# Kernel optimization log

Measured on AMD Instinct MI355X. Metric: run time of the kernel, lower is better.

## Reference

```python
import jax, jax.numpy as jnp
import numpy as np

# graph sizes: G graphs of N_PER nodes each (block-diagonal batched graph)
G, N_PER, F, NHID, E_PER = 128, 512, 128, 128, 4096
N = G * N_PER
E = G * E_PER
L1, L2, L3 = 4, 2, 2            # PANConv filter sizes (conv1 uses init filter_size=4)
K1, K2, K3 = N_PER // 2, N_PER // 4, N_PER // 8  # ratio=0.5 top-k per pooling stage


def setup_inputs() -> dict:
    ks = jax.random.split(jax.random.key(0), 10)
    rng = np.random.default_rng(0)
    off = (np.arange(G) * N_PER)[:, None]
    src = (rng.integers(0, N_PER, size=(G, E_PER)) + off).reshape(-1)
    dst = (rng.integers(0, N_PER, size=(G, E_PER)) + off).reshape(-1)
    edge_index = jnp.asarray(np.stack([src, dst]).astype(np.int32))
    batch = jnp.repeat(jnp.arange(G, dtype=jnp.int32), N_PER)
    def w(k, shp, fan):
        return jax.random.normal(k, shp, jnp.float32) / np.float32(np.sqrt(fan))
    z = lambda *s: jnp.zeros(s, jnp.float32)
    return dict(
        x=jax.random.normal(ks[0], (N, F), jnp.float32),
        edge_index=edge_index, batch=batch,
        lump_W=w(ks[1], (F, NHID), F), lump_b=z(NHID),
        conv1_W=w(ks[2], (NHID, NHID), NHID), conv1_b=z(NHID),
        conv2_W=w(ks[3], (NHID, NHID), NHID), conv2_b=z(NHID),
        conv3_W=w(ks[4], (NHID, NHID), NHID), conv3_b=z(NHID),
        pool1_p=w(ks[5], (NHID,), NHID), pool1_beta=jnp.full((2,), 0.5, jnp.float32),
        pool2_p=w(ks[6], (NHID,), NHID), pool2_beta=jnp.full((2,), 0.5, jnp.float32),
        pool3_p=w(ks[7], (NHID,), NHID), pool3_beta=jnp.full((2,), 0.5, jnp.float32),
        lin1_W=w(ks[8], (NHID, NHID // 2), NHID), lin1_b=z(NHID // 2),
        lin2_W=w(ks[9], (NHID // 2, 1), NHID // 2), lin2_b=z(1),
    )


def _pan_prop(h, src, dst, ew, L):
    # (sum_{l=0..L} A^l) @ h, A weighted by edge weights ew, via iterated gather/scatter
    acc, y = h, h
    n = h.shape[0]
    for _ in range(L):
        y = jax.ops.segment_sum(y[src] * ew[:, None], dst, num_segments=n)
        acc = acc + y
    return acc


def _pan_conv(x, src, dst, ew, W, b, L):
    # PANConv: M = Z^{-1/2} (sum_{l<=L} A^l) Z^{-1/2};  out = M x W + b
    d = _pan_prop(jnp.ones((x.shape[0], 1), x.dtype), src, dst, ew, L)[:, 0]
    dinv = jax.lax.rsqrt(jnp.maximum(d, 1e-12))
    h = dinv[:, None] * _pan_prop(dinv[:, None] * x, src, dst, ew, L)
    return h @ W + b


def _pan_pool(x, src, dst, ew, p, beta, n_per, k):
    # PANPooling: score = beta0*(x.p)/||p|| + beta1*node_strength; per-graph top-k
    n = x.shape[0]
    deg = jax.ops.segment_sum(ew, dst, num_segments=n)
    score = beta[0] * (x @ p) / jnp.linalg.norm(p) + beta[1] * deg
    _, idx = jax.lax.top_k(score.reshape(G, n_per), k)          # [G, k] local indices
    perm = (idx + (jnp.arange(G) * n_per)[:, None]).reshape(-1)  # [G*k] global
    x_new = x[perm] * jnp.tanh(score[perm])[:, None]
    inv = jnp.zeros((n,), jnp.int32).at[perm].set(jnp.arange(G * k, dtype=jnp.int32))
    mask = jnp.zeros((n,), x.dtype).at[perm].set(1.0)
    # keep edge arrays fixed-size: dropped edges get weight 0 (same math as filtering)
    return x_new, inv[src], inv[dst], ew * mask[src] * mask[dst], perm


def reference(x, edge_index, batch, lump_W, lump_b, conv1_W, conv1_b, conv2_W, conv2_b,
              conv3_W, conv3_b, pool1_p, pool1_beta, pool2_p, pool2_beta, pool3_p,
              pool3_beta, lin1_W, lin1_b, lin2_W, lin2_b):
    src, dst = edge_index[0], edge_index[1]
    ew = jnp.ones((src.shape[0],), x.dtype)
    h = x @ lump_W + lump_b                                   # PANLump lift
    h = _pan_conv(h, src, dst, ew, conv1_W, conv1_b, L1)
    h, src, dst, ew, perm1 = _pan_pool(h, src, dst, ew, pool1_p, pool1_beta, N_PER, K1)
    h = _pan_conv(h, src, dst, ew, conv2_W, conv2_b, L2)
    h, src, dst, ew, perm2 = _pan_pool(h, src, dst, ew, pool2_p, pool2_beta, K1, K2)
    h = _pan_conv(h, src, dst, ew, conv3_W, conv3_b, L3)
    h, src, dst, ew, perm3 = _pan_pool(h, src, dst, ew, pool3_p, pool3_beta, K2, K3)
    seg = jnp.repeat(jnp.arange(G, dtype=jnp.int32), K3)
    mean = jax.ops.segment_sum(h, seg, num_segments=G) / jnp.float32(K3)  # scatter_mean
    out = jax.nn.relu(mean @ lin1_W + lin1_b) @ lin2_W + lin2_b           # [G, 1]
    return out
```

## Files before the change

### kernel.cpp

```cpp
#include <hip/hip_runtime.h>
#include <math.h>

#define G_     128
#define E_     524288
#define EPG    4096
#define DEGMAX 48

typedef __attribute__((ext_vector_type(8))) short bf16x8;
typedef __attribute__((ext_vector_type(4))) float f32x4;
typedef __attribute__((ext_vector_type(4))) unsigned short u16x4;

__device__ inline void split_bf16(float x, short& hi, short& lo){
    unsigned u = __float_as_uint(x);
    hi = (short)(u >> 16);
    float hf = __uint_as_float(u & 0xffff0000u);
    unsigned r = __float_as_uint(x - hf);
    lo = (short)(r >> 16);
}

__device__ inline int ysw(int v, int f4){ return v*32 + (f4 ^ ((v & 7) << 2)); }

template<int WAVES>
__device__ void gemm_body(char* smem, int bid, const float* __restrict__ X,
        const float* __restrict__ W, const float* __restrict__ bias, float* __restrict__ Y,
        const float* __restrict__ p, const float* __restrict__ beta,
        const int* __restrict__ cntv, float* __restrict__ score){
    short* wsh = (short*)smem;
    short* wsl = (short*)(smem + 34816);
    float* bsh = (float*)(smem + 69632);
    float* qs  = (float*)(smem + 70144);
    float* rednorm = (float*)(smem + 70656);
    const int NT = WAVES*64;
    int t = threadIdx.x;
    for (int e = t; e < 16384; e += NT){
        int k = e >> 7, n = e & 127;
        short hi, lo; split_bf16(W[e], hi, lo);
        wsh[n*136 + k] = hi; wsl[n*136 + k] = lo;
    }
    if (t < 128) bsh[t] = bias[t];
    if (score && t < 64){ float a = p[t], b = p[t+64]; rednorm[t] = a*a + b*b; }
    __syncthreads();
    float b1 = 0.f;
    if (score){
        if (t == 0){ float s = 0.f; for (int i = 0; i < 64; i++) s += rednorm[i]; rednorm[0] = sqrtf(s); }
        __syncthreads();
        if (t < 128) qs[t] = beta[0] * p[t] / rednorm[0];
        b1 = beta[1];
        __syncthreads();
    }
    int wave = t >> 6, lane = t & 63;
    int ln = lane & 15, q = lane >> 4;
    size_t rb = (size_t)bid * (WAVES*16);
    const float* xrow = &X[(rb + wave*16 + ln)*128 + q*8];
    f32x4 acc[8];
    #pragma unroll
    for (int i = 0; i < 8; i++) acc[i] = (f32x4){0.f,0.f,0.f,0.f};
    #pragma unroll
    for (int kc = 0; kc < 4; kc++){
        float4 xa = *(const float4*)(xrow + kc*32);
        float4 xb = *(const float4*)(xrow + kc*32 + 4);
        bf16x8 ah, al; short hi, lo;
        split_bf16(xa.x, hi, lo); ah[0]=hi; al[0]=lo;
        split_bf16(xa.y, hi, lo); ah[1]=hi; al[1]=lo;
        split_bf16(xa.z, hi, lo); ah[2]=hi; al[2]=lo;
        split_bf16(xa.w, hi, lo); ah[3]=hi; al[3]=lo;
        split_bf16(xb.x, hi, lo); ah[4]=hi; al[4]=lo;
        split_bf16(xb.y, hi, lo); ah[5]=hi; al[5]=lo;
        split_bf16(xb.z, hi, lo); ah[6]=hi; al[6]=lo;
        split_bf16(xb.w, hi, lo); ah[7]=hi; al[7]=lo;
        #pragma unroll
        for (int nt = 0; nt < 8; nt++){
            int wo = (nt*16 + ln)*136 + kc*32 + q*8;
            bf16x8 bh = *(const bf16x8*)&wsh[wo];
            bf16x8 bl = *(const bf16x8*)&wsl[wo];
            acc[nt] = __builtin_amdgcn_mfma_f32_16x16x32_bf16(ah, bh, acc[nt], 0, 0, 0);
            acc[nt] = __builtin_amdgcn_mfma_f32_16x16x32_bf16(ah, bl, acc[nt], 0, 0, 0);
            acc[nt] = __builtin_amdgcn_mfma_f32_16x16x32_bf16(al, bh, acc[nt], 0, 0, 0);
        }
    }
    #pragma unroll
    for (int nt = 0; nt < 8; nt++){
        int c = nt*16 + ln;
        float bb = bsh[c];
        #pragma unroll
        for (int r = 0; r < 4; r++){
            Y[(rb + wave*16 + q*4 + r)*128 + c] = acc[nt][r] + bb;
        }
    }
    if (score){
        #pragma unroll
        for (int r = 0; r < 4; r++){
            float sp = 0.f;
            #pragma unroll
            for (int nt = 0; nt < 8; nt++){
                int c = nt*16 + ln;
                sp += (acc[nt][r] + bsh[c]) * qs[c];
            }
            sp += __shfl_xor(sp, 1);
            sp += __shfl_xor(sp, 2);
            sp += __shfl_xor(sp, 4);
            sp += __shfl_xor(sp, 8);
            if (ln == 0){
                int row = (int)rb + wave*16 + q*4 + r;
                score[row] = sp + b1 * (float)cntv[row];
            }
        }
    }
}

template<int WAVES>
__global__ __launch_bounds__(WAVES*64) void k_gemm_mfma(const float* __restrict__ X,
        const float* __restrict__ W, const float* __restrict__ bias, float* __restrict__ Y,
        const float* __restrict__ p, const float* __restrict__ beta,
        const int* __restrict__ cntv, float* __restrict__ score){
    __shared__ __align__(16) char smem[70912];
    gemm_body<WAVES>(smem, blockIdx.x, X, W, bias, Y, p, beta, cntv, score);
}

__global__ __launch_bounds__(512) void k_prep1(const int* __restrict__ ei,
        int* __restrict__ cnt, unsigned short* __restrict__ csrcp,
        int* __restrict__ permg, float* __restrict__ dinvg){
    __shared__ int   lcnt[512];
    __shared__ __align__(16) unsigned short csrS[512*DEGMAX + 8];
    __shared__ float y[1024];
    __shared__ int   bins[64];
    __shared__ int   permS[512];
    int g = blockIdx.x, t = threadIdx.x, gbase = g*512;
    lcnt[t] = 0;
    if (t < 64) bins[t] = 0;
    unsigned* c32 = (unsigned*)csrS;
    for (int i = t; i < 512*DEGMAX/2 + 4; i += 512) c32[i] = 0;
    __syncthreads();
    for (int i = t; i < EPG; i += 512){
        int e = g*EPG + i;
        int sv = ei[e] & 511;
        int d  = ei[E_ + e] & 511;
        int slot = atomicAdd(&lcnt[d], 1);
        if (slot < DEGMAX) csrS[d*DEGMAX + slot] = (unsigned short)sv;
    }
    __syncthreads();
    {
        unsigned* dst = (unsigned*)(csrcp + (size_t)gbase*DEGMAX);
        for (int i = t; i < 512*DEGMAX/2; i += 512) dst[i] = c32[i];
    }
    int rawc = lcnt[t];
    cnt[gbase + t] = rawc;
    int dc = min(rawc, DEGMAX);
    atomicAdd(&bins[dc], 1);
    __syncthreads();
    if (t < 64){
        int v0 = bins[t], s = v0;
        #pragma unroll
        for (int off = 1; off < 64; off <<= 1){
            int n = __shfl_up(s, off);
            if (t >= off) s += n;
        }
        bins[t] = s - v0;
    }
    __syncthreads();
    {
        int slot = atomicAdd(&bins[dc], 1);
        int pk = t | (dc << 16);
        permS[slot] = pk;
        permg[gbase + slot] = pk;
    }
    __syncthreads();
    int pk = permS[t];
    int pv = pk & 0xffff, pd = pk >> 16;
    y[pv] = 1.f;
    __syncthreads();
    float dacc = 1.f;
    int cur = 0;
    for (int l = 0; l < 4; l++){
        const float* la = &y[cur*512];
        float s = 0.f;
        int nq = (pd + 3) >> 2;
        const u16x4* cp = (const u16x4*)(csrS + pv*DEGMAX);
        u16x4 oc = cp[0];
        #pragma unroll 1
        for (int jq = 0; jq < nq; jq++){
            u16x4 ocn = cp[jq + 1];
            s += (la[(int)oc[0]] + la[(int)oc[1]]) + (la[(int)oc[2]] + la[(int)oc[3]]);
            oc = ocn;
        }
        if (nq) s -= (float)(nq*4 - pd) * la[0];
        y[(1^cur)*512 + pv] = s;
        dacc += s;
        __syncthreads();
        cur ^= 1;
    }
    dinvg[gbase + pv] = rsqrtf(fmaxf(dacc, 1e-12f));
}

template<int NPER, int L, int IT, bool SEL>
__global__ __launch_bounds__(1024)
void k_prop(const int* __restrict__ permg, const float* __restrict__ dinvg,
        const unsigned short* __restrict__ csrcp,
        const float* __restrict__ X, const int* __restrict__ selg,
        const float* __restrict__ thg, float* __restrict__ OUT){
    __shared__ __align__(16) float y[NPER*32];
    __shared__ float dinvs[NPER];
    int g = blockIdx.x, fq = blockIdx.y, gbase = g*NPER;
    int t = threadIdx.x;
    int f4 = (t & 7)*4;
    int fo = fq*32 + f4;
    if (t < NPER) dinvs[t] = dinvg[gbase + t];
    int pkr[IT];
    {
        int wv = t >> 6, gi = (t >> 3) & 7;
        #pragma unroll
        for (int it = 0; it < IT; it++){
            int ch = (it & 1) ? (15 - wv) : wv;
            pkr[it] = permg[gbase + (16*it + ch)*8 + gi];
        }
    }
    __syncthreads();
    float4 acc[IT];
    #pragma unroll
    for (int it = 0; it < IT; it++){
        int v = pkr[it] & 0xffff;
        float d = dinvs[v];
        size_t row;
        if (SEL){
            row = (size_t)selg[gbase + v];
            d *= thg[gbase + v];
        } else {
            row = (size_t)(gbase + v);
        }
        float4 w = *(const float4*)&X[row*128 + fo];
        w.x*=d; w.y*=d; w.z*=d; w.w*=d;
        acc[it] = w;
        *(float4*)&y[ysw(v, f4)] = w;
    }
    __syncthreads();
    for (int l = 0; l < L; l++){
        float4 s[IT];
        #pragma unroll
        for (int it = 0; it < IT; it++){
            int pk = pkr[it];
            int c = pk >> 16;
            int nq = (c + 3) >> 2;
            const u16x4* cp = (const u16x4*)(csrcp + (size_t)(gbase + (pk & 0xffff))*DEGMAX);
            float4 ss = make_float4(0.f,0.f,0.f,0.f);
            u16x4 oc = cp[0];
            #pragma unroll 1
            for (int jq = 0; jq < nq; jq++){
                u16x4 ocn = cp[jq + 1];
                float4 w0 = *(const float4*)&y[ysw((int)oc[0], f4)];
                float4 w1 = *(const float4*)&y[ysw((int)oc[1], f4)];
                float4 w2 = *(const float4*)&y[ysw((int)oc[2], f4)];
                float4 w3 = *(const float4*)&y[ysw((int)oc[3], f4)];
                ss.x += (w0.x + w1.x) + (w2.x + w3.x);
                ss.y += (w0.y + w1.y) + (w2.y + w3.y);
                ss.z += (w0.z + w1.z) + (w2.z + w3.z);
                ss.w += (w0.w + w1.w) + (w2.w + w3.w);
                oc = ocn;
            }
            if (nq){
                float fp = (float)(nq*4 - c);
                float4 z = *(const float4*)&y[f4];
                ss.x -= fp*z.x; ss.y -= fp*z.y; ss.z -= fp*z.z; ss.w -= fp*z.w;
            }
            s[it] = ss;
        }
        __syncthreads();
        #pragma unroll
        for (int it = 0; it < IT; it++){
            int v = pkr[it] & 0xffff;
            *(float4*)&y[ysw(v, f4)] = s[it];
            acc[it].x+=s[it].x; acc[it].y+=s[it].y; acc[it].z+=s[it].z; acc[it].w+=s[it].w;
        }
        __syncthreads();
    }
    #pragma unroll
    for (int it = 0; it < IT; it++){
        int v = pkr[it] & 0xffff;
        float d = dinvs[v];
        float4 w = acc[it];
        w.x*=d; w.y*=d; w.z*=d; w.w*=d;
        *(float4*)&OUT[(size_t)(gbase + v)*128 + fo] = w;
    }
}

template<int NPER, bool BUILD>
__global__ __launch_bounds__(512) void k_pooltop(const float* __restrict__ score_in,
        const int* __restrict__ esrc_in, const int* __restrict__ edst_in,
        int* __restrict__ esrc_out, int* __restrict__ edst_out,
        int* __restrict__ cnt_next, unsigned short* __restrict__ csrcp,
        int* __restrict__ permg, float* __restrict__ dinvg,
        int* __restrict__ selg, float* __restrict__ thg){
    const int K = NPER/2;
    constexpr int CSRSZ = BUILD ? (NPER/2)*DEGMAX + 8 : 8;
    __shared__ __align__(16) float sc[NPER];
    __shared__ int  nid[NPER];
    __shared__ int  lcnt[NPER/2];
    __shared__ int  bins[64];
    __shared__ int  permS[NPER/2];
    __shared__ __align__(16) unsigned short csrS[CSRSZ];
    int g = blockIdx.x, t = threadIdx.x, gbase = g*NPER;
    if (t < K) lcnt[t] = 0;
    if (t < 64) bins[t] = 0;
    if (BUILD){
        unsigned* c32 = (unsigned*)csrS;
        for (int i = t; i < K*DEGMAX/2 + 4; i += 512) c32[i] = 0;
    }
    if (t < NPER) sc[t] = score_in[gbase + t];
    __syncthreads();
    if (t < NPER){
        float s = sc[t];
        int rank = 0;
        const float4* sc4 = (const float4*)sc;
        #pragma unroll 8
        for (int j4 = 0; j4 < NPER/4; j4++){
            float4 v = sc4[j4];
            int j = j4*4;
            rank += (v.x > s) || (v.x == s && (j+0) < t);
            rank += (v.y > s) || (v.y == s && (j+1) < t);
            rank += (v.z > s) || (v.z == s && (j+2) < t);
            rank += (v.w > s) || (v.w == s && (j+3) < t);
        }
        if (rank < K){
            nid[t] = g*K + rank;
            selg[g*K + rank] = gbase + t;
            thg[g*K + rank]  = tanhf(s);
        } else nid[t] = -1;
    }
    __syncthreads();
    if (BUILD){
        for (int i = t; i < EPG; i += 512){
            int e = g*EPG + i;
            int d = edst_in[e];
            if (d < 0) continue;
            int s_ = esrc_in[e];
            int ns = nid[s_ - gbase], nd = nid[d - gbase];
            if ((ns | nd) < 0){ edst_out[e] = -1; }
            else {
                esrc_out[e] = ns; edst_out[e] = nd;
                int ndl = nd & (K-1);
                int slot = atomicAdd(&lcnt[ndl], 1);
                if (slot < DEGMAX) csrS[ndl*DEGMAX + slot] = (unsigned short)(ns & (K-1));
            }
        }
        __syncthreads();
        {
            unsigned* c32 = (unsigned*)csrS;
            unsigned* dst = (unsigned*)(csrcp + (size_t)g*K*DEGMAX);
            for (int i = t; i < K*DEGMAX/2; i += 512) dst[i] = c32[i];
        }
        float* yd = sc;
        int rawc = 0, dc = 0;
        if (t < K){
            rawc = lcnt[t];
            cnt_next[g*K + t] = rawc;
            dc = min(rawc, DEGMAX);
            atomicAdd(&bins[dc], 1);
        }
        __syncthreads();
        if (t < 64){
            int v0 = bins[t], s = v0;
            #pragma unroll
            for (int off = 1; off < 64; off <<= 1){
                int n = __shfl_up(s, off);
                if (t >= off) s += n;
            }
            bins[t] = s - v0;
        }
        __syncthreads();
        if (t < K){
            int slot = atomicAdd(&bins[dc], 1);
            permS[slot] = t | (dc << 16);
            permg[g*K + slot] = permS[slot];
        }
        __syncthreads();
        int pv = 0, pd = 0;
        if (t < K){
            int pk = permS[t];
            pv = pk & 0xffff; pd = pk >> 16;
            yd[pv] = 1.f;
        }
        __syncthreads();
        float dacc = 1.f;
        int cur = 0;
        for (int l = 0; l < 2; l++){
            if (t < K){
                const float* la = &yd[cur*K];
                float s = 0.f;
                int nq = (pd + 3) >> 2;
                const u16x4* cp = (const u16x4*)(csrS + pv*DEGMAX);
                u16x4 oc = cp[0];
                #pragma unroll 1
                for (int jq = 0; jq < nq; jq++){
                    u16x4 ocn = cp[jq + 1];
                    s += (la[(int)oc[0]] + la[(int)oc[1]]) + (la[(int)oc[2]] + la[(int)oc[3]]);
                    oc = ocn;
                }
                if (nq) s -= (float)(nq*4 - pd) * la[0];
                yd[(1^cur)*K + pv] = s;
                dacc += s;
            }
            __syncthreads();
            cur ^= 1;
        }
        if (t < K) dinvg[g*K + pv] = rsqrtf(fmaxf(dacc, 1e-12f));
    }
}

__global__ __launch_bounds__(512) void k_stage3(const float* __restrict__ X,
        const float* __restrict__ W, const float* __restrict__ bias,
        const float* __restrict__ p, const float* __restrict__ beta,
        const int* __restrict__ cntv,
        const float* __restrict__ W1, const float* __restrict__ b1,
        const float* __restrict__ W2, const float* __restrict__ b2,
        float* __restrict__ out){
    __shared__ __align__(16) char smem[70912];
    __shared__ float scs[128];
    __shared__ float thS[64];
    __shared__ int   selS[64];
    __shared__ float mr[128];
    short* wsh = (short*)smem;
    short* wsl = (short*)(smem + 34816);
    float* bsh = (float*)(smem + 69632);
    float* qs  = (float*)(smem + 70144);
    float* rednorm = (float*)(smem + 70656);
    int g = blockIdx.x, t = threadIdx.x;
    for (int e = t; e < 16384; e += 512){
        int k = e >> 7, n = e & 127;
        short hi, lo; split_bf16(W[e], hi, lo);
        wsh[n*136 + k] = hi; wsl[n*136 + k] = lo;
    }
    if (t < 128) bsh[t] = bias[t];
    if (t < 64){ float a = p[t], b = p[t+64]; rednorm[t] = a*a + b*b; }
    __syncthreads();
    if (t == 0){ float s = 0.f; for (int i = 0; i < 64; i++) s += rednorm[i]; rednorm[0] = sqrtf(s); }
    __syncthreads();
    if (t < 128) qs[t] = beta[0] * p[t] / rednorm[0];
    float b1v = beta[1];
    __syncthreads();
    int wave = t >> 6, lane = t & 63;
    int ln = lane & 15, q = lane >> 4;
    const float* xrow = &X[((size_t)g*128 + wave*16 + ln)*128 + q*8];
    f32x4 acc[8];
    #pragma unroll
    for (int i = 0; i < 8; i++) acc[i] = (f32x4){0.f,0.f,0.f,0.f};
    #pragma unroll
    for (int kc = 0; kc < 4; kc++){
        float4 xa = *(const float4*)(xrow + kc*32);
        float4 xb = *(const float4*)(xrow + kc*32 + 4);
        bf16x8 ah, al; short hi, lo;
        split_bf16(xa.x, hi, lo); ah[0]=hi; al[0]=lo;
        split_bf16(xa.y, hi, lo); ah[1]=hi; al[1]=lo;
        split_bf16(xa.z, hi, lo); ah[2]=hi; al[2]=lo;
        split_bf16(xa.w, hi, lo); ah[3]=hi; al[3]=lo;
        split_bf16(xb.x, hi, lo); ah[4]=hi; al[4]=lo;
        split_bf16(xb.y, hi, lo); ah[5]=hi; al[5]=lo;
        split_bf16(xb.z, hi, lo); ah[6]=hi; al[6]=lo;
        split_bf16(xb.w, hi, lo); ah[7]=hi; al[7]=lo;
        #pragma unroll
        for (int nt = 0; nt < 8; nt++){
            int wo = (nt*16 + ln)*136 + kc*32 + q*8;
            bf16x8 bh = *(const bf16x8*)&wsh[wo];
            bf16x8 bl = *(const bf16x8*)&wsl[wo];
            acc[nt] = __builtin_amdgcn_mfma_f32_16x16x32_bf16(ah, bh, acc[nt], 0, 0, 0);
            acc[nt] = __builtin_amdgcn_mfma_f32_16x16x32_bf16(ah, bl, acc[nt], 0, 0, 0);
            acc[nt] = __builtin_amdgcn_mfma_f32_16x16x32_bf16(al, bh, acc[nt], 0, 0, 0);
        }
    }
    #pragma unroll
    for (int r = 0; r < 4; r++){
        float sp = 0.f;
        #pragma unroll
        for (int nt = 0; nt < 8; nt++){
            int c = nt*16 + ln;
            sp += (acc[nt][r] + bsh[c]) * qs[c];
        }
        sp += __shfl_xor(sp, 1);
        sp += __shfl_xor(sp, 2);
        sp += __shfl_xor(sp, 4);
        sp += __shfl_xor(sp, 8);
        if (ln == 0){
            int rl = wave*16 + q*4 + r;
            scs[rl] = sp + b1v * (float)cntv[g*128 + rl];
        }
    }
    __syncthreads();
    float* Yl = (float*)smem;
    #pragma unroll
    for (int nt = 0; nt < 8; nt++){
        int c = nt*16 + ln;
        float bb = bsh[c];
        #pragma unroll
        for (int r = 0; r < 4; r++){
            Yl[(wave*16 + q*4 + r)*132 + c] = acc[nt][r] + bb;
        }
    }
    __syncthreads();
    if (t < 128){
        float s = scs[t];
        int rank = 0;
        const float4* sc4 = (const float4*)scs;
        #pragma unroll 8
        for (int j4 = 0; j4 < 32; j4++){
            float4 v = sc4[j4];
            int j = j4*4;
            rank += (v.x > s) || (v.x == s && (j+0) < t);
            rank += (v.y > s) || (v.y == s && (j+1) < t);
            rank += (v.z > s) || (v.z == s && (j+2) < t);
            rank += (v.w > s) || (v.w == s && (j+3) < t);
        }
        if (rank < 64){ selS[rank] = t; thS[rank] = tanhf(s); }
    }
    __syncthreads();
    if (t < 128){
        float s = 0.f;
        #pragma unroll 8
        for (int r = 0; r < 64; r++) s += Yl[selS[r]*132 + t] * thS[r];
        mr[t] = s * (1.f/64.f);
    }
    __syncthreads();
    if (t < 64){
        float a = b1[t];
        #pragma unroll 8
        for (int k = 0; k < 128; k++) a += mr[k]*W1[k*64 + t];
        a = fmaxf(a, 0.f);
        float r = a * W2[t];
        #pragma unroll
        for (int off = 32; off > 0; off >>= 1) r += __shfl_down(r, off);
        if (t == 0) out[g] = r + b2[0];
    }
}

extern "C" void kernel_launch(void* const* d_in, const int* in_sizes, int n_in,
                              void* d_out, int out_size, void* d_ws, size_t ws_size,
                              hipStream_t stream){
    (void)in_sizes; (void)n_in; (void)out_size; (void)ws_size;
    const float* x     = (const float*)d_in[0];
    const int*   ei    = (const int*)d_in[1];
    const float* lumpW = (const float*)d_in[3];
    const float* lumpb = (const float*)d_in[4];
    const float* convW[3]    = {(const float*)d_in[5], (const float*)d_in[7], (const float*)d_in[9]};
    const float* convB[3]    = {(const float*)d_in[6], (const float*)d_in[8], (const float*)d_in[10]};
    const float* poolP[3]    = {(const float*)d_in[11], (const float*)d_in[13], (const float*)d_in[15]};
    const float* poolBeta[3] = {(const float*)d_in[12], (const float*)d_in[14], (const float*)d_in[16]};
    const float* lin1W = (const float*)d_in[17];
    const float* lin1b = (const float*)d_in[18];
    const float* lin2W = (const float*)d_in[19];
    const float* lin2b = (const float*)d_in[20];
    float* out = (float*)d_out;

    char* w8 = (char*)d_ws;
    size_t off = 0;
    auto alloc = [&](size_t bytes)->char*{
        char* p = w8 + off; off += (bytes + 255) & ~(size_t)255; return p;
    };
    float* A     = (float*)alloc((size_t)65536*128*4);
    float* Bb    = (float*)alloc((size_t)65536*128*4);
    int*   srcA  = (int*)alloc((size_t)E_*4);
    int*   dstA  = (int*)alloc((size_t)E_*4);
    unsigned short* csr1 = (unsigned short*)alloc((size_t)65536*DEGMAX*2);
    unsigned short* csr2 = (unsigned short*)alloc((size_t)32768*DEGMAX*2);
    unsigned short* csr3 = (unsigned short*)alloc((size_t)16384*DEGMAX*2);
    int*   cntA  = (int*)alloc((size_t)(65536+32768+16384)*4);
    int*   cnt1 = cntA, *cnt2 = cntA + 65536, *cnt3 = cntA + 98304;
    int*   perm1 = (int*)alloc((size_t)65536*4);
    int*   perm2 = (int*)alloc((size_t)32768*4);
    int*   perm3 = (int*)alloc((size_t)16384*4);
    float* dinv1 = (float*)alloc((size_t)65536*4);
    float* dinv2 = (float*)alloc((size_t)32768*4);
    float* dinv3 = (float*)alloc((size_t)16384*4);
    float* score1 = (float*)alloc((size_t)65536*4);
    float* score2 = (float*)alloc((size_t)32768*4);
    int*   sel2  = (int*)alloc((size_t)32768*4);
    int*   sel3  = (int*)alloc((size_t)16384*4);
    float* th2   = (float*)alloc((size_t)32768*4);
    float* th3   = (float*)alloc((size_t)16384*4);

    k_prep1<<<G_, 512, 0, stream>>>(ei, cnt1, csr1, perm1, dinv1);
    k_gemm_mfma<8><<<512, 512, 0, stream>>>(x, lumpW, lumpb, A,
            nullptr, nullptr, nullptr, nullptr);

    k_prop<512,4,4,false><<<dim3(G_,4), 1024, 0, stream>>>(perm1, dinv1, csr1, A,
            nullptr, nullptr, Bb);
    k_gemm_mfma<8><<<512, 512, 0, stream>>>(Bb, convW[0], convB[0], A,
            poolP[0], poolBeta[0], cnt1, score1);
    k_pooltop<512,true><<<G_, 512, 0, stream>>>(score1, ei, ei + E_, srcA, dstA,
            cnt2, csr2, perm2, dinv2, sel2, th2);

    k_prop<256,2,2,true><<<dim3(G_,4), 1024, 0, stream>>>(perm2, dinv2, csr2, A,
            sel2, th2, Bb);
    k_gemm_mfma<8><<<256, 512, 0, stream>>>(Bb, convW[1], convB[1], A,
            poolP[1], poolBeta[1], cnt2, score2);
    k_pooltop<256,true><<<G_, 512, 0, stream>>>(score2, srcA, dstA, srcA, dstA,
            cnt3, csr3, perm3, dinv3, sel3, th3);

    k_prop<128,2,1,true><<<dim3(G_,4), 1024, 0, stream>>>(perm3, dinv3, csr3, A,
            sel3, th3, Bb);
    k_stage3<<<G_, 512, 0, stream>>>(Bb, convW[2], convB[2],
            poolP[2], poolBeta[2], cnt3, lin1W, lin1b, lin2W, lin2b, out);
}
```

Measured before the change: 284.1 us.

## Pre-split GEMM weights into bf16 hi/lo once and drop LDS swizzle in prop

Adds a small kernel that converts each 128x128 weight matrix into transposed bf16 hi/lo halves once per call. The GEMM and stage3 kernels then copy these into shared memory instead of having every block redo the split and transpose. The XOR swizzle on the prop kernel's shared feature buffer is also removed to save index arithmetic. This adds one extra launch and a global buffer, and may raise LDS bank conflicts in the gather loop.

```diff
diff --git a/kernel.cpp b/kernel.cpp
--- a/kernel.cpp
+++ b/kernel.cpp
@@ -18,11 +18,24 @@
     lo = (short)(r >> 16);
 }
 
-__device__ inline int ysw(int v, int f4){ return v*32 + (f4 ^ ((v & 7) << 2)); }
+__global__ __launch_bounds__(256) void k_splitW(const float* __restrict__ W0,
+        const float* __restrict__ W1, const float* __restrict__ W2,
+        const float* __restrict__ W3, unsigned short* __restrict__ outw){
+    int mat = blockIdx.x >> 3, blk = blockIdx.x & 7;
+    const float* W = (mat==0)?W0:(mat==1)?W1:(mat==2)?W2:W3;
+    unsigned short* hi = outw + (size_t)mat*2*17408;
+    unsigned short* lo = hi + 17408;
+    for (int e = blk*256 + threadIdx.x; e < 16384; e += 2048){
+        int k = e >> 7, n = e & 127;
+        short h, l; split_bf16(W[e], h, l);
+        hi[n*136 + k] = h; lo[n*136 + k] = l;
+    }
+}
 
 template<int WAVES>
 __device__ void gemm_body(char* smem, int bid, const float* __restrict__ X,
-        const float* __restrict__ W, const float* __restrict__ bias, float* __restrict__ Y,
+        const unsigned short* __restrict__ Wsp, const float* __restrict__ bias,
+        float* __restrict__ Y,
         const float* __restrict__ p, const float* __restrict__ beta,
         const int* __restrict__ cntv, float* __restrict__ score){
     short* wsh = (short*)smem;
@@ -32,10 +45,12 @@
     float* rednorm = (float*)(smem + 70656);
     const int NT = WAVES*64;
     int t = threadIdx.x;
-    for (int e = t; e < 16384; e += NT){
-        int k = e >> 7, n = e & 127;
-        short hi, lo; split_bf16(W[e], hi, lo);
-        wsh[n*136 + k] = hi; wsl[n*136 + k] = lo;
+    {
+        const unsigned* h32 = (const unsigned*)Wsp;
+        const unsigned* l32 = (const unsigned*)(Wsp + 17408);
+        unsigned* wsh32 = (unsigned*)wsh;
+        unsigned* wsl32 = (unsigned*)wsl;
+        for (int i = t; i < 8704; i += NT){ wsh32[i] = h32[i]; wsl32[i] = l32[i]; }
     }
     if (t < 128) bsh[t] = bias[t];
     if (score && t < 64){ float a = p[t], b = p[t+64]; rednorm[t] = a*a + b*b; }
@@ -110,11 +125,12 @@
 
 template<int WAVES>
 __global__ __launch_bounds__(WAVES*64) void k_gemm_mfma(const float* __restrict__ X,
-        const float* __restrict__ W, const float* __restrict__ bias, float* __restrict__ Y,
+        const unsigned short* __restrict__ Wsp, const float* __restrict__ bias,
+        float* __restrict__ Y,
         const float* __restrict__ p, const float* __restrict__ beta,
         const int* __restrict__ cntv, float* __restrict__ score){
     __shared__ __align__(16) char smem[70912];
-    gemm_body<WAVES>(smem, blockIdx.x, X, W, bias, Y, p, beta, cntv, score);
+    gemm_body<WAVES>(smem, blockIdx.x, X, Wsp, bias, Y, p, beta, cntv, score);
 }
 
 __global__ __launch_bounds__(512) void k_prep1(const int* __restrict__ ei,
@@ -230,7 +246,7 @@
         float4 w = *(const float4*)&X[row*128 + fo];
         w.x*=d; w.y*=d; w.z*=d; w.w*=d;
         acc[it] = w;
-        *(float4*)&y[ysw(v, f4)] = w;
+        *(float4*)&y[v*32 + f4] = w;
     }
     __syncthreads();
     for (int l = 0; l < L; l++){
@@ -246,10 +262,10 @@
             #pragma unroll 1
             for (int jq = 0; jq < nq; jq++){
                 u16x4 ocn = cp[jq + 1];
-                float4 w0 = *(const float4*)&y[ysw((int)oc[0], f4)];
-                float4 w1 = *(const float4*)&y[ysw((int)oc[1], f4)];
-                float4 w2 = *(const float4*)&y[ysw((int)oc[2], f4)];
-                float4 w3 = *(const float4*)&y[ysw((int)oc[3], f4)];
+                float4 w0 = *(const float4*)&y[((int)oc[0])*32 + f4];
+                float4 w1 = *(const float4*)&y[((int)oc[1])*32 + f4];
+                float4 w2 = *(const float4*)&y[((int)oc[2])*32 + f4];
+                float4 w3 = *(const float4*)&y[((int)oc[3])*32 + f4];
                 ss.x += (w0.x + w1.x) + (w2.x + w3.x);
                 ss.y += (w0.y + w1.y) + (w2.y + w3.y);
                 ss.z += (w0.z + w1.z) + (w2.z + w3.z);
@@ -267,7 +283,7 @@
         #pragma unroll
         for (int it = 0; it < IT; it++){
             int v = pkr[it] & 0xffff;
-            *(float4*)&y[ysw(v, f4)] = s[it];
+            *(float4*)&y[v*32 + f4] = s[it];
             acc[it].x+=s[it].x; acc[it].y+=s[it].y; acc[it].z+=s[it].z; acc[it].w+=s[it].w;
         }
         __syncthreads();
@@ -406,7 +422,7 @@
 }
 
 __global__ __launch_bounds__(512) void k_stage3(const float* __restrict__ X,
-        const float* __restrict__ W, const float* __restrict__ bias,
+        const unsigned short* __restrict__ Wsp, const float* __restrict__ bias,
         const float* __restrict__ p, const float* __restrict__ beta,
         const int* __restrict__ cntv,
         const float* __restrict__ W1, const float* __restrict__ b1,
@@ -423,10 +439,12 @@
     float* qs  = (float*)(smem + 70144);
     float* rednorm = (float*)(smem + 70656);
     int g = blockIdx.x, t = threadIdx.x;
-    for (int e = t; e < 16384; e += 512){
-        int k = e >> 7, n = e & 127;
-        short hi, lo; split_bf16(W[e], hi, lo);
-        wsh[n*136 + k] = hi; wsl[n*136 + k] = lo;
+    {
+        const unsigned* h32 = (const unsigned*)Wsp;
+        const unsigned* l32 = (const unsigned*)(Wsp + 17408);
+        unsigned* wsh32 = (unsigned*)wsh;
+        unsigned* wsl32 = (unsigned*)wsl;
+        for (int i = t; i < 8704; i += 512){ wsh32[i] = h32[i]; wsl32[i] = l32[i]; }
     }
     if (t < 128) bsh[t] = bias[t];
     if (t < 64){ float a = p[t], b = p[t+64]; rednorm[t] = a*a + b*b; }
@@ -573,27 +591,33 @@
     int*   sel3  = (int*)alloc((size_t)16384*4);
     float* th2   = (float*)alloc((size_t)32768*4);
     float* th3   = (float*)alloc((size_t)16384*4);
-
+    unsigned short* wsp = (unsigned short*)alloc((size_t)4*2*17408*2);
+    unsigned short* wspLump = wsp;
+    unsigned short* wspC0   = wsp + 1*2*17408;
+    unsigned short* wspC1   = wsp + 2*2*17408;
+    unsigned short* wspC2   = wsp + 3*2*17408;
+
+    k_splitW<<<32, 256, 0, stream>>>(lumpW, convW[0], convW[1], convW[2], wsp);
     k_prep1<<<G_, 512, 0, stream>>>(ei, cnt1, csr1, perm1, dinv1);
-    k_gemm_mfma<8><<<512, 512, 0, stream>>>(x, lumpW, lumpb, A,
+    k_gemm_mfma<8><<<512, 512, 0, stream>>>(x, wspLump, lumpb, A,
             nullptr, nullptr, nullptr, nullptr);
 
     k_prop<512,4,4,false><<<dim3(G_,4), 1024, 0, stream>>>(perm1, dinv1, csr1, A,
             nullptr, nullptr, Bb);
-    k_gemm_mfma<8><<<512, 512, 0, stream>>>(Bb, convW[0], convB[0], A,
+    k_gemm_mfma<8><<<512, 512, 0, stream>>>(Bb, wspC0, convB[0], A,
             poolP[0], poolBeta[0], cnt1, score1);
     k_pooltop<512,true><<<G_, 512, 0, stream>>>(score1, ei, ei + E_, srcA, dstA,
             cnt2, csr2, perm2, dinv2, sel2, th2);
 
     k_prop<256,2,2,true><<<dim3(G_,4), 1024, 0, stream>>>(perm2, dinv2, csr2, A,
             sel2, th2, Bb);
-    k_gemm_mfma<8><<<256, 512, 0, stream>>>(Bb, convW[1], convB[1], A,
+    k_gemm_mfma<8><<<256, 512, 0, stream>>>(Bb, wspC1, convB[1], A,
             poolP[1], poolBeta[1], cnt2, score2);
     k_pooltop<256,true><<<G_, 512, 0, stream>>>(score2, srcA, dstA, srcA, dstA,
             cnt3, csr3, perm3, dinv3, sel3, th3);
 
     k_prop<128,2,1,true><<<dim3(G_,4), 1024, 0, stream>>>(perm3, dinv3, csr3, A,
             sel3, th3, Bb);
-    k_stage3<<<G_, 512, 0, stream>>>(Bb, convW[2], convB[2],
+    k_stage3<<<G_, 512, 0, stream>>>(Bb, wspC2, convB[2],
             poolP[2], poolBeta[2], cnt3, lin1W, lin1b, lin2W, lin2b, out);
 }
```

Measured after the change: 273.9 us. 3.6% less time.
